# Optimization experiments

Hardware: AMD Instinct MI355X
Metric: run time of the kernel (lower is better)

The kernel has to match this reference:

```python
import jax, jax.numpy as jnp
import numpy as np

B, T, D, P = 32, 2048, 256, 100000
MAX_SPAN = 16


def setup_inputs() -> dict:
    key = jax.random.key(0)
    k0, k1, k2, k3, k4, k5 = jax.random.split(key, 6)
    token_embs = jax.random.normal(k0, (B, T, D), dtype=jnp.float32)
    p1_span = jax.random.randint(k1, (P,), 1, MAX_SPAN + 1, dtype=jnp.int32)
    p2_span = jax.random.randint(k2, (P,), 1, MAX_SPAN + 1, dtype=jnp.int32)
    p1_start = jax.random.randint(k3, (P,), 0, T - MAX_SPAN, dtype=jnp.int32)
    p2_start = jax.random.randint(k4, (P,), 0, T - MAX_SPAN, dtype=jnp.int32)
    pair_batch = jax.random.randint(k5, (P,), 0, B, dtype=jnp.int32)
    return {
        "token_embs": token_embs,
        "p1_start": p1_start,
        "p1_span": p1_span,
        "p2_start": p2_start,
        "p2_span": p2_span,
        "pair_batch": pair_batch,
    }


def reference(token_embs, p1_start, p1_span, p2_start, p2_span, pair_batch):
    # token_embs: [B, T, D]; per-pair ranges [start, start+span) within batch row pair_batch.
    # Range mean via exclusive prefix sums: mean = (csum[end] - csum[start]) / span.
    b, t, d = token_embs.shape
    csum = jnp.concatenate(
        [jnp.zeros((b, 1, d), token_embs.dtype), jnp.cumsum(token_embs, axis=1)],
        axis=1,
    )  # [B, T+1, D]

    def span_mean(start, span):
        end = start + span
        s = csum[pair_batch, end] - csum[pair_batch, start]  # [P, D]
        return s / span[:, None].astype(token_embs.dtype)

    p1 = span_mean(p1_start, p1_span)
    p2 = span_mean(p2_start, p2_span)
    return jnp.concatenate([p1, p2], axis=-1)  # [P, 2D]
```

## Files before the change

### kernel.cpp

```cpp
#include <hip/hip_runtime.h>


#define PB_B 32
#define PB_T 2048
#define PB_TP1 2049
#define PB_D 256
#define PB_P 100000
#define CHUNK 32
#define NCHUNK (PB_T / CHUNK)

__global__ __launch_bounds__(256) void chunk_sum_kernel(
    const float* __restrict__ emb, float* __restrict__ cs)
{
    const int wid  = blockIdx.x * 4 + (threadIdx.x >> 6);
    const int lane = threadIdx.x & 63;
    const int b = wid >> 6;
    const int c = wid & (NCHUNK - 1);

    const float4* __restrict__ src =
        (const float4*)(emb + ((long long)b * PB_T + c * CHUNK) * PB_D) + lane;
    float4 acc = make_float4(0.f, 0.f, 0.f, 0.f);
    #pragma unroll
    for (int t = 0; t < CHUNK; ++t) {
        float4 v = src[t * (PB_D / 4)];
        acc.x += v.x; acc.y += v.y; acc.z += v.z; acc.w += v.w;
    }
    ((float4*)(cs + ((long long)b * NCHUNK + c) * PB_D))[lane] = acc;
}

__global__ __launch_bounds__(256) void chunk_scan_kernel(float* __restrict__ cs)
{
    const int b = blockIdx.x;
    const int d = threadIdx.x;
    float run = 0.f;
    #pragma unroll
    for (int c = 0; c < NCHUNK; ++c) {
        float* p = cs + ((long long)b * NCHUNK + c) * PB_D + d;
        float v = *p;
        *p = run;
        run += v;
    }
}

__global__ __launch_bounds__(256) void csum_write_kernel(
    const float* __restrict__ emb, const float* __restrict__ cs,
    float* __restrict__ csum)
{
    const int wid  = blockIdx.x * 4 + (threadIdx.x >> 6);
    const int lane = threadIdx.x & 63;
    const int b = wid >> 6;
    const int c = wid & (NCHUNK - 1);

    float4 acc = ((const float4*)(cs + ((long long)b * NCHUNK + c) * PB_D))[lane];
    const float4* __restrict__ src =
        (const float4*)(emb + ((long long)b * PB_T + c * CHUNK) * PB_D) + lane;
    float4* __restrict__ dst =
        (float4*)(csum + ((long long)b * PB_TP1 + c * CHUNK + 1) * PB_D) + lane;

    if (c == 0) {
        ((float4*)(csum + (long long)b * PB_TP1 * PB_D))[lane] =
            make_float4(0.f, 0.f, 0.f, 0.f);
    }
    #pragma unroll
    for (int t = 0; t < CHUNK; ++t) {
        float4 v = src[t * (PB_D / 4)];
        acc.x += v.x; acc.y += v.y; acc.z += v.z; acc.w += v.w;
        dst[t * (PB_D / 4)] = acc;
    }
}

__global__ __launch_bounds__(256) void gather_kernel(
    const float* __restrict__ csum,
    const int* __restrict__ p1_start, const int* __restrict__ p1_span,
    const int* __restrict__ p2_start, const int* __restrict__ p2_span,
    const int* __restrict__ pair_batch,
    float* __restrict__ out)
{
    const int pair = blockIdx.x * 4 + (threadIdx.x >> 6);
    const int lane = threadIdx.x & 63;
    if (pair >= PB_P) return;

    const int b  = pair_batch[pair];
    const int s1 = p1_start[pair], n1 = p1_span[pair];
    const int s2 = p2_start[pair], n2 = p2_span[pair];

    const float* base = csum + (long long)b * PB_TP1 * PB_D;
    float4 e1 = ((const float4*)(base + (long long)(s1 + n1) * PB_D))[lane];
    float4 b1 = ((const float4*)(base + (long long)s1 * PB_D))[lane];
    float4 e2 = ((const float4*)(base + (long long)(s2 + n2) * PB_D))[lane];
    float4 b2 = ((const float4*)(base + (long long)s2 * PB_D))[lane];

    const float i1 = 1.f / (float)n1;
    const float i2 = 1.f / (float)n2;
    float4 r1 = make_float4((e1.x - b1.x) * i1, (e1.y - b1.y) * i1,
                            (e1.z - b1.z) * i1, (e1.w - b1.w) * i1);
    float4 r2 = make_float4((e2.x - b2.x) * i2, (e2.y - b2.y) * i2,
                            (e2.z - b2.z) * i2, (e2.w - b2.w) * i2);

    float4* o = (float4*)(out + (long long)pair * (2 * PB_D));
    o[lane]      = r1;
    o[64 + lane] = r2;
}

__global__ __launch_bounds__(256) void pair_mean_direct(
    const float* __restrict__ token_embs,
    const int* __restrict__ p1_start, const int* __restrict__ p1_span,
    const int* __restrict__ p2_start, const int* __restrict__ p2_span,
    const int* __restrict__ pair_batch,
    float* __restrict__ out)
{
    const int wave = threadIdx.x >> 6;
    const int lane = threadIdx.x & 63;
    const long long task = (long long)blockIdx.x * 4 + wave;
    if (task >= 2LL * PB_P) return;
    const int pair = (int)(task >> 1);
    const int half = (int)(task & 1);
    const int b     = pair_batch[pair];
    const int start = half ? p2_start[pair] : p1_start[pair];
    const int span  = half ? p2_span[pair]  : p1_span[pair];
    const float4* src =
        (const float4*)(token_embs + ((long long)b * PB_T + start) * PB_D) + lane;
    float4 acc = make_float4(0.f, 0.f, 0.f, 0.f);
    #pragma unroll 4
    for (int t = 0; t < span; ++t) {
        float4 v = src[(long long)t * (PB_D / 4)];
        acc.x += v.x; acc.y += v.y; acc.z += v.z; acc.w += v.w;
    }
    const float inv = 1.0f / (float)span;
    float4* dst = (float4*)(out + (long long)pair * (2 * PB_D) + half * PB_D) + lane;
    *dst = make_float4(acc.x * inv, acc.y * inv, acc.z * inv, acc.w * inv);
}

extern "C" void kernel_launch(void* const* d_in, const int* in_sizes, int n_in,
                              void* d_out, int out_size, void* d_ws, size_t ws_size,
                              hipStream_t stream) {
    const float* token_embs = (const float*)d_in[0];
    const int* p1_start = (const int*)d_in[1];
    const int* p1_span  = (const int*)d_in[2];
    const int* p2_start = (const int*)d_in[3];
    const int* p2_span  = (const int*)d_in[4];
    const int* pair_batch = (const int*)d_in[5];
    float* out = (float*)d_out;

    const size_t csum_elems = (size_t)PB_B * PB_TP1 * PB_D;
    const size_t cs_elems   = (size_t)PB_B * NCHUNK * PB_D;
    const size_t need_bytes = (csum_elems + cs_elems) * sizeof(float);

    if (ws_size < need_bytes) {
        pair_mean_direct<<<(2 * PB_P + 3) / 4, 256, 0, stream>>>(
            token_embs, p1_start, p1_span, p2_start, p2_span, pair_batch, out);
        return;
    }

    float* csum = (float*)d_ws;
    float* cs   = csum + csum_elems;

    const int nwave_bc = PB_B * NCHUNK;
    chunk_sum_kernel<<<nwave_bc / 4, 256, 0, stream>>>(token_embs, cs);
    chunk_scan_kernel<<<PB_B, 256, 0, stream>>>(cs);
    csum_write_kernel<<<nwave_bc / 4, 256, 0, stream>>>(token_embs, cs, csum);
    gather_kernel<<<(PB_P + 3) / 4, 256, 0, stream>>>(
        csum, p1_start, p1_span, p2_start, p2_span, pair_batch, out);
}
```

Baseline: 338.6 us.

## Sort pairs by batch row and swizzle gather blocks for cache locality

Adds a counting sort (histogram, scan, scatter) that groups pair indices by batch row. The gather kernel then walks that permutation, with a block-index swizzle that spreads work across the 8 XCDs, so pairs sharing a batch's csum rows hit in L2. It also doubles CHUNK to 64 with partial unrolling and drops the small-workspace fallback. The cost is four extra small launches, scattered output writes and indirect index loads.

```diff
diff --git a/kernel.cpp b/kernel.cpp
--- a/kernel.cpp
+++ b/kernel.cpp
@@ -6,7 +6,7 @@
 #define PB_TP1 2049
 #define PB_D 256
 #define PB_P 100000
-#define CHUNK 32
+#define CHUNK 64
 #define NCHUNK (PB_T / CHUNK)
 
 __global__ __launch_bounds__(256) void chunk_sum_kernel(
@@ -14,13 +14,13 @@
 {
     const int wid  = blockIdx.x * 4 + (threadIdx.x >> 6);
     const int lane = threadIdx.x & 63;
-    const int b = wid >> 6;
+    const int b = wid >> 5;
     const int c = wid & (NCHUNK - 1);
 
     const float4* __restrict__ src =
         (const float4*)(emb + ((long long)b * PB_T + c * CHUNK) * PB_D) + lane;
     float4 acc = make_float4(0.f, 0.f, 0.f, 0.f);
-    #pragma unroll
+    #pragma unroll 8
     for (int t = 0; t < CHUNK; ++t) {
         float4 v = src[t * (PB_D / 4)];
         acc.x += v.x; acc.y += v.y; acc.z += v.z; acc.w += v.w;
@@ -48,7 +48,7 @@
 {
     const int wid  = blockIdx.x * 4 + (threadIdx.x >> 6);
     const int lane = threadIdx.x & 63;
-    const int b = wid >> 6;
+    const int b = wid >> 5;
     const int c = wid & (NCHUNK - 1);
 
     float4 acc = ((const float4*)(cs + ((long long)b * NCHUNK + c) * PB_D))[lane];
@@ -61,7 +61,7 @@
         ((float4*)(csum + (long long)b * PB_TP1 * PB_D))[lane] =
             make_float4(0.f, 0.f, 0.f, 0.f);
     }
-    #pragma unroll
+    #pragma unroll 8
     for (int t = 0; t < CHUNK; ++t) {
         float4 v = src[t * (PB_D / 4)];
         acc.x += v.x; acc.y += v.y; acc.z += v.z; acc.w += v.w;
@@ -69,17 +69,60 @@
     }
 }
 
+__global__ __launch_bounds__(256) void hist_kernel(
+    const int* __restrict__ pair_batch, int* __restrict__ counts)
+{
+    __shared__ int l_cnt[PB_B];
+    if (threadIdx.x < PB_B) l_cnt[threadIdx.x] = 0;
+    __syncthreads();
+    const int i = blockIdx.x * 256 + threadIdx.x;
+    if (i < PB_P) atomicAdd(&l_cnt[pair_batch[i]], 1);
+    __syncthreads();
+    if (threadIdx.x < PB_B && l_cnt[threadIdx.x] > 0)
+        atomicAdd(&counts[threadIdx.x], l_cnt[threadIdx.x]);
+}
+
+__global__ void scan_counts_kernel(const int* __restrict__ counts,
+                                   int* __restrict__ cursors)
+{
+    if (threadIdx.x == 0 && blockIdx.x == 0) {
+        int run = 0;
+        #pragma unroll
+        for (int b = 0; b < PB_B; ++b) { cursors[b] = run; run += counts[b]; }
+    }
+}
+
+__global__ __launch_bounds__(256) void scatter_kernel(
+    const int* __restrict__ pair_batch, int* __restrict__ cursors,
+    int* __restrict__ perm)
+{
+    __shared__ int l_cnt[PB_B];
+    __shared__ int l_base[PB_B];
+    if (threadIdx.x < PB_B) l_cnt[threadIdx.x] = 0;
+    __syncthreads();
+    const int i = blockIdx.x * 256 + threadIdx.x;
+    int b = 0, lpos = 0;
+    const bool valid = (i < PB_P);
+    if (valid) { b = pair_batch[i]; lpos = atomicAdd(&l_cnt[b], 1); }
+    __syncthreads();
+    if (threadIdx.x < PB_B && l_cnt[threadIdx.x] > 0)
+        l_base[threadIdx.x] = atomicAdd(&cursors[threadIdx.x], l_cnt[threadIdx.x]);
+    __syncthreads();
+    if (valid) perm[l_base[b] + lpos] = i;
+}
+
 __global__ __launch_bounds__(256) void gather_kernel(
-    const float* __restrict__ csum,
+    const float* __restrict__ csum, const int* __restrict__ perm,
     const int* __restrict__ p1_start, const int* __restrict__ p1_span,
     const int* __restrict__ p2_start, const int* __restrict__ p2_span,
     const int* __restrict__ pair_batch,
     float* __restrict__ out)
 {
-    const int pair = blockIdx.x * 4 + (threadIdx.x >> 6);
+    const int pos_block = (blockIdx.x & 7) * (25000 / 8) + (blockIdx.x >> 3);
+    const int pos = pos_block * 4 + (threadIdx.x >> 6);
     const int lane = threadIdx.x & 63;
-    if (pair >= PB_P) return;
 
+    const int pair = perm[pos];
     const int b  = pair_batch[pair];
     const int s1 = p1_start[pair], n1 = p1_span[pair];
     const int s2 = p2_start[pair], n2 = p2_span[pair];
@@ -102,35 +145,6 @@
     o[64 + lane] = r2;
 }
 
-__global__ __launch_bounds__(256) void pair_mean_direct(
-    const float* __restrict__ token_embs,
-    const int* __restrict__ p1_start, const int* __restrict__ p1_span,
-    const int* __restrict__ p2_start, const int* __restrict__ p2_span,
-    const int* __restrict__ pair_batch,
-    float* __restrict__ out)
-{
-    const int wave = threadIdx.x >> 6;
-    const int lane = threadIdx.x & 63;
-    const long long task = (long long)blockIdx.x * 4 + wave;
-    if (task >= 2LL * PB_P) return;
-    const int pair = (int)(task >> 1);
-    const int half = (int)(task & 1);
-    const int b     = pair_batch[pair];
-    const int start = half ? p2_start[pair] : p1_start[pair];
-    const int span  = half ? p2_span[pair]  : p1_span[pair];
-    const float4* src =
-        (const float4*)(token_embs + ((long long)b * PB_T + start) * PB_D) + lane;
-    float4 acc = make_float4(0.f, 0.f, 0.f, 0.f);
-    #pragma unroll 4
-    for (int t = 0; t < span; ++t) {
-        float4 v = src[(long long)t * (PB_D / 4)];
-        acc.x += v.x; acc.y += v.y; acc.z += v.z; acc.w += v.w;
-    }
-    const float inv = 1.0f / (float)span;
-    float4* dst = (float4*)(out + (long long)pair * (2 * PB_D) + half * PB_D) + lane;
-    *dst = make_float4(acc.x * inv, acc.y * inv, acc.z * inv, acc.w * inv);
-}
-
 extern "C" void kernel_launch(void* const* d_in, const int* in_sizes, int n_in,
                               void* d_out, int out_size, void* d_ws, size_t ws_size,
                               hipStream_t stream) {
@@ -144,21 +158,24 @@
 
     const size_t csum_elems = (size_t)PB_B * PB_TP1 * PB_D;
     const size_t cs_elems   = (size_t)PB_B * NCHUNK * PB_D;
-    const size_t need_bytes = (csum_elems + cs_elems) * sizeof(float);
-
-    if (ws_size < need_bytes) {
-        pair_mean_direct<<<(2 * PB_P + 3) / 4, 256, 0, stream>>>(
-            token_embs, p1_start, p1_span, p2_start, p2_span, pair_batch, out);
-        return;
-    }
 
     float* csum = (float*)d_ws;
     float* cs   = csum + csum_elems;
+    int* counts  = (int*)(cs + cs_elems);
+    int* cursors = counts + PB_B;
+    int* perm    = cursors + PB_B;
 
     const int nwave_bc = PB_B * NCHUNK;
     chunk_sum_kernel<<<nwave_bc / 4, 256, 0, stream>>>(token_embs, cs);
     chunk_scan_kernel<<<PB_B, 256, 0, stream>>>(cs);
     csum_write_kernel<<<nwave_bc / 4, 256, 0, stream>>>(token_embs, cs, csum);
-    gather_kernel<<<(PB_P + 3) / 4, 256, 0, stream>>>(
-        csum, p1_start, p1_span, p2_start, p2_span, pair_batch, out);
+
+    hipMemsetAsync(counts, 0, PB_B * sizeof(int), stream);
+    const int hb = (PB_P + 255) / 256;
+    hist_kernel<<<hb, 256, 0, stream>>>(pair_batch, counts);
+    scan_counts_kernel<<<1, 64, 0, stream>>>(counts, cursors);
+    scatter_kernel<<<hb, 256, 0, stream>>>(pair_batch, cursors, perm);
+
+    gather_kernel<<<PB_P / 4, 256, 0, stream>>>(
+        csum, perm, p1_start, p1_span, p2_start, p2_span, pair_batch, out);
 }
```

Result: no change. 337.6 us (-0.3%).
